# Optimization experiments

Hardware: AMD Instinct MI355X
Metric: run time of the kernel (lower is better)

## Reference

```python
import jax, jax.numpy as jnp
import numpy as np

D_MODEL = 1024
N_QK = 32
D_QK = 32
N_OV = 2048
D_OV = 1
SEQ = 1024
BATCH = 2
VKV = 16
ROT_DIM = 32
ROT_BASE = 10000.0
SCALE = D_QK ** 0.5  # cfg.attn_scale default = sqrt(d_qk_head)


def _kaiming(k, shape, fan_in):
    # torch kaiming_normal_(mode='fan_in', nonlinearity='relu'): std = sqrt(2/fan_in)
    return jax.random.normal(k, shape, jnp.float32) * np.sqrt(2.0 / fan_in)


def setup_inputs() -> dict:
    key = jax.random.key(0)
    ks = jax.random.split(key, 7)
    return {
        'resid': jax.random.normal(ks[0], (BATCH, SEQ, D_MODEL), jnp.float32),
        'W_Q': _kaiming(ks[1], (N_QK, D_MODEL, D_QK), D_MODEL * D_QK),
        'W_K': _kaiming(ks[2], (N_QK, D_MODEL, D_QK), D_MODEL * D_QK),
        'W_V': _kaiming(ks[3], (N_OV, D_MODEL, D_OV), D_MODEL * D_OV),
        'W_O': _kaiming(ks[4], (N_OV, D_OV, D_MODEL), D_OV * D_MODEL),
        'b_Q': jnp.zeros((N_QK, D_QK), jnp.float32),
        'b_K': jnp.zeros((N_QK, D_QK), jnp.float32),
        'b_V': jnp.zeros((N_OV, D_OV), jnp.float32),
        'virtual_k': _kaiming(ks[5], (VKV, N_QK, D_QK), N_QK * D_QK),
        'virtual_v': jnp.zeros((VKV, N_OV, D_OV), jnp.float32),
    }


def _rotary_sin_cos(n_ctx, rd, base):
    # GPT-NeoX style (non-adjacent pairs): freq repeated as (2 d)
    pos = jnp.arange(n_ctx, dtype=jnp.float32)
    dim = jnp.arange(rd // 2, dtype=jnp.float32)
    freq = base ** (dim / (rd / 2))
    freq = jnp.concatenate([freq, freq])
    angles = pos[:, None] / freq[None, :]  # (n_ctx, rd)
    return jnp.sin(angles), jnp.cos(angles)


def _apply_rotary(x, sin, cos, rd):
    # x: (batch, seq, head, d_head)
    s = x.shape[1]
    x_rot, x_pass = x[..., :rd], x[..., rd:]
    flip = jnp.concatenate([-x_rot[..., rd // 2:], x_rot[..., :rd // 2]], axis=-1)
    rot = x_rot * cos[None, :s, None, :] + flip * sin[None, :s, None, :]
    return jnp.concatenate([rot, x_pass], axis=-1)


def reference(resid, W_Q, W_K, W_V, W_O, b_Q, b_K, b_V, virtual_k, virtual_v):
    b, s, _ = resid.shape
    # per-head QKV projections + biases
    q = jnp.einsum('bsm,hmd->bshd', resid, W_Q) + b_Q  # (b,s,n_qk,d_qk)
    k = jnp.einsum('bsm,hmd->bshd', resid, W_K) + b_K
    v = jnp.einsum('bsm,hmd->bshd', resid, W_V) + b_V  # (b,s,n_ov,d_ov)
    sin, cos = _rotary_sin_cos(s, ROT_DIM, ROT_BASE)
    q = _apply_rotary(q, sin, cos, ROT_DIM)
    k = _apply_rotary(k, sin, cos, ROT_DIM)
    # append virtual KV at the end of the key axis
    k = jnp.concatenate([k, jnp.broadcast_to(virtual_k[None], (b,) + virtual_k.shape)], axis=1)
    v = jnp.concatenate([v, jnp.broadcast_to(virtual_v[None], (b,) + virtual_v.shape)], axis=1)
    kv_len = s + VKV
    scores = jnp.einsum('bqhd,bkhd->bhqk', q, k) / SCALE
    # causal mask: tril(ones(n_ctx, n_ctx+vkv), diagonal=vkv)
    mask = jnp.arange(kv_len)[None, :] <= (jnp.arange(s)[:, None] + VKV)
    scores = jnp.where(mask[None, None], scores, -jnp.inf)
    pattern = jax.nn.softmax(scores, axis=-1)
    pattern = jnp.where(jnp.isnan(pattern), 0.0, pattern)
    # repeat_interleave of pattern over ov heads == grouping v per qk head
    ratio = N_OV // N_QK
    v_g = v.reshape(b, kv_len, N_QK, ratio * D_OV)
    z = jnp.einsum('bhqk,bkhr->bqhr', pattern, v_g)  # (b,s,n_qk,ratio*d_ov)
    z = z.reshape(b, s, N_OV, D_OV)
    out = jnp.einsum('bqhd,hdm->bqm', z, W_O)  # cal_out: no b_O
    return out
```

## Files before the change

### kernel.cpp

```cpp
#include <hip/hip_runtime.h>
#include <hip/hip_bf16.h>
#include <math.h>


typedef short bf16x8 __attribute__((ext_vector_type(8)));
typedef short short4v __attribute__((ext_vector_type(4)));
typedef float f32x4 __attribute__((ext_vector_type(4)));
typedef int int4v __attribute__((ext_vector_type(4)));
typedef __hip_bfloat16 bf16;

#define AS1(p) ((const __attribute__((address_space(1))) void*)(const void*)(p))
#define AS3(p) ((__attribute__((address_space(3))) void*)(void*)(p))

static constexpr float INV_SCALE = 0.17677669529663687f;

__device__ inline short rnd_bf16(float x) {
  unsigned u = __float_as_uint(x);
  return (short)((u + 0x7fffu + ((u >> 16) & 1u)) >> 16);
}

__device__ inline int pack_bf16_pair(float hi, float lo) {
  unsigned a = __float_as_uint(hi) + 0x8000u;
  unsigned b = __float_as_uint(lo) + 0x8000u;
  return (int)__builtin_amdgcn_perm(a, b, 0x07060302u);
}

__global__ __launch_bounds__(256) void prep(
    const float* __restrict__ resid, const float* __restrict__ WV,
    const float* __restrict__ WQ, const float* __restrict__ WK,
    const float* __restrict__ WO, const float* __restrict__ vk,
    const float* __restrict__ vv,
    bf16* __restrict__ A_bf, bf16* __restrict__ Wt, bf16* __restrict__ Wot,
    bf16* __restrict__ Kb, bf16* __restrict__ Vb) {
  __shared__ float t[64][65];
  const int blk = blockIdx.x, tid = threadIdx.x;
  if (blk < 4096) {
    const float* src = (blk < 2048) ? resid : WV;
    short* dst = (short*)((blk < 2048) ? A_bf : (Wt + (size_t)2048 * 1024));
    int i = ((blk & 2047) * 256 + tid) * 4;
    float4 v = *(const float4*)(src + i);
    dst[i + 0] = rnd_bf16(v.x); dst[i + 1] = rnd_bf16(v.y);
    dst[i + 2] = rnd_bf16(v.z); dst[i + 3] = rnd_bf16(v.w);
  } else if (blk < 7168) {
    int idx = (blk - 4096) * 256 + tid;
    if (idx < 262144) {
      int b = idx >> 17, rem = idx & 131071;
      int j = rem >> 10, c = rem & 1023;
      int h = c >> 5, d = c & 31;
      float v = (j < 16) ? vk[j * 1024 + c] : 0.f;
      Kb[(((size_t)(b * 32 + h)) * 1152 + 1024 + j) * 32 + d] = __float2bfloat16(v);
    } else if (idx < 524288) {
      int i2 = idx - 262144;
      int b = i2 >> 17, rem = i2 & 131071;
      int ch = rem >> 6, p = rem & 63;
      int pl = p & 31;
      int u = (p & 32) | ((pl & 4) << 2) | ((pl & 24) >> 1) | (pl & 3);
      float v = (u < 16) ? vv[(size_t)u * 2048 + ch] : 0.f;
      int hv = ch >> 6, c = ch & 63;
      int slot = c * 8 + ((p >> 3) ^ (c & 7));
      Vb[((((size_t)(b * 32 + hv)) * 17 + 16) * 512 + slot) * 8 + (p & 7)] = __float2bfloat16(v);
    }
  } else if (blk < 8192) {
    int i = blk - 7168;
    int mt = i & 15, h = (i >> 4) & 31, qk = i >> 9;
    const float* W = qk ? WK : WQ;
    const int m0 = mt * 64;
    for (int idx = tid; idx < 64 * 32; idx += 256) {
      int ii = idx >> 5, d = idx & 31;
      t[ii][d] = W[((size_t)h * 1024 + m0 + ii) * 32 + d];
    }
    __syncthreads();
    const int rowbase = qk * 1024 + h * 32;
    for (int idx = tid; idx < 32 * 64; idx += 256) {
      int d = idx >> 6, ii = idx & 63;
      Wt[(size_t)(rowbase + d) * 1024 + m0 + ii] = __float2bfloat16(t[ii][d]);
    }
  } else {
    int i = blk - 8192;
    int h0 = (i & 31) * 64, m0 = (i >> 5) * 64;
    for (int idx = tid; idx < 64 * 64; idx += 256) {
      int ii = idx >> 6, j = idx & 63;
      t[ii][j] = WO[(size_t)(h0 + ii) * 1024 + m0 + j];
    }
    __syncthreads();
    for (int idx = tid; idx < 64 * 64; idx += 256) {
      int ii = idx >> 6, j = idx & 63;
      Wot[(size_t)(m0 + ii) * 2048 + h0 + j] = __float2bfloat16(t[j][ii]);
    }
  }
}

__global__ __launch_bounds__(256) void gemm1_fused(
    const bf16* __restrict__ A, const bf16* __restrict__ Bt,
    const float* __restrict__ bQ, const float* __restrict__ bK,
    const float* __restrict__ bV,
    bf16* __restrict__ Qb, bf16* __restrict__ Kb, bf16* __restrict__ Vb) {
  __shared__ __align__(16) short As[128 * 32];
  __shared__ __align__(16) short Bs[128 * 32];
  const int tileM = blockIdx.y * 128, tileN = blockIdx.x * 128;
  const int tid = threadIdx.x, wave = tid >> 6, lane = tid & 63;
  const int wm = (wave >> 1) * 64, wn = (wave & 1) * 64;
  const int mrow = lane & 15, kq = lane >> 4;
  f32x4 acc[4][4] = {};

  for (int k0 = 0; k0 < 1024; k0 += 32) {
#pragma unroll
    for (int i = 0; i < 2; i++) {
      int c = (wave * 2 + i) * 64 + lane;
      int row = c >> 2, ko = (c & 3) * 8;
      const short* ga = (const short*)A + (size_t)(tileM + row) * 1024 + k0 + ko;
      const short* gb = (const short*)Bt + (size_t)(tileN + row) * 1024 + k0 + ko;
      __builtin_amdgcn_global_load_lds(AS1(ga), AS3(&As[(wave * 2 + i) * 512]), 16, 0, 0);
      __builtin_amdgcn_global_load_lds(AS1(gb), AS3(&Bs[(wave * 2 + i) * 512]), 16, 0, 0);
    }
    __syncthreads();
    bf16x8 af[4], bfr[4];
#pragma unroll
    for (int t = 0; t < 4; t++) {
      af[t]  = *(const bf16x8*)&As[(wm + t * 16 + mrow) * 32 + kq * 8];
      bfr[t] = *(const bf16x8*)&Bs[(wn + t * 16 + mrow) * 32 + kq * 8];
    }
#pragma unroll
    for (int i = 0; i < 4; i++)
#pragma unroll
      for (int j = 0; j < 4; j++)
        acc[i][j] = __builtin_amdgcn_mfma_f32_16x16x32_bf16(af[i], bfr[j], acc[i][j], 0, 0, 0);
    __syncthreads();
  }

  const int col = lane & 15, rq = lane >> 4;
  if (tileN < 2048) {
    const int qk = tileN >> 10;
    const float* bias = qk ? bK : bQ;
    const int hA = ((tileN & 1023) + wn) >> 5;
    const float b0a = bias[hA * 32 + col],        b1a = bias[hA * 32 + col + 16];
    const float b0b = bias[(hA + 1) * 32 + col],  b1b = bias[(hA + 1) * 32 + col + 16];
    const float invf = exp2f(col * -0.8304820237218406f);
#pragma unroll
    for (int i = 0; i < 4; i++)
#pragma unroll
      for (int r = 0; r < 4; r++) {
        int mg = tileM + wm + i * 16 + rq * 4 + r;
        int s = mg & 1023, bb = mg >> 10;
        float sv, cv;
        __sincosf((float)s * invf, &sv, &cv);
#pragma unroll
        for (int p = 0; p < 2; p++) {
          float x0 = acc[i][2 * p][r]     + (p ? b0b : b0a);
          float x1 = acc[i][2 * p + 1][r] + (p ? b1b : b1a);
          float y0 = x0 * cv - x1 * sv, y1 = x1 * cv + x0 * sv;
          int h = hA + p;
          if (qk == 0) {
            short* q = (short*)Qb + (((size_t)(bb * 32 + h)) * 1024 + s) * 32 + col;
            q[0]  = rnd_bf16(y0 * INV_SCALE);
            q[16] = rnd_bf16(y1 * INV_SCALE);
          } else {
            short* kp = (short*)Kb + (((size_t)(bb * 32 + h)) * 1152 + s) * 32 + col;
            kp[0]  = rnd_bf16(y0);
            kp[16] = rnd_bf16(y1);
          }
        }
      }
  } else {
    const int hv = (tileN - 2048 + wn) >> 6;
#pragma unroll
    for (int i = 0; i < 4; i++)
#pragma unroll
      for (int j = 0; j < 4; j++) {
        int c = j * 16 + col;
        float bias = bV[hv * 64 + c];
        int m0 = tileM + wm + i * 16 + rq * 4;
        int s0 = m0 & 1023, bb = m0 >> 10;
        int chunk = s0 >> 6, w = s0 & 63, u0 = w & 31;
        int p0 = (u0 & 3) | ((u0 & 16) >> 2) | ((u0 & 8) << 1) | ((u0 & 4) << 1);
        int p = (w & 32) | p0;
        int slot = c * 8 + ((p >> 3) ^ (c & 7));
        short4v s4;
#pragma unroll
        for (int r = 0; r < 4; r++) s4[r] = rnd_bf16(acc[i][j][r] + bias);
        *(short4v*)((short*)Vb +
            ((((size_t)(bb * 32 + hv)) * 17 + chunk) * 512 + slot) * 8 + (p & 7)) = s4;
      }
  }
}

__global__ __launch_bounds__(256) void attn_mfma(
    const bf16* __restrict__ Qb, const bf16* __restrict__ Kb,
    const bf16* __restrict__ Vb, bf16* __restrict__ Zb) {
  __shared__ __align__(16) short Vs[4][4096];
  const int flat = blockIdx.x;
  const int xcd = flat & 7, jj = flat >> 3;
  const int hqb = xcd * 8 + (jj & 7);
  const int x = jj >> 3;
  const int hq = hqb & 31, b = hqb >> 5;
  const int wave = threadIdx.x >> 6, lane = threadIdx.x & 63;
  const int col = lane & 15, quad = lane >> 4;
  const int t = (wave == 0) ? x : (wave == 1) ? 31 - x : (wave == 2) ? 32 + x : 63 - x;
  const int qw = t * 16;

  const bf16x8 qf = *(const bf16x8*)((const short*)Qb +
      (((size_t)(b * 32 + hq)) * 1024 + qw + col) * 32 + quad * 8);
  const short* kbase = (const short*)Kb + ((size_t)(b * 32 + hq)) * 1152 * 32 + quad * 8;
  const short* vbh = (const short*)Vb + ((size_t)(b * 32 + hq)) * (17 * 4096) + lane * 8;
  short* vdst = &Vs[wave][0];

  const int kend = (qw + 32 < 1040) ? qw + 32 : 1040;
  const int nch = (kend + 63) >> 6;

  f32x4 O[4] = {};
  float m = -1e30f, l = 0.f;

  bf16x8 kf[4];
#pragma unroll
  for (int mbk = 0; mbk < 4; mbk++)
    kf[mbk] = *(const bf16x8*)(kbase + (size_t)(mbk * 16 + col) * 32);
#pragma unroll
  for (int g = 0; g < 8; g++)
    __builtin_amdgcn_global_load_lds(AS1(vbh + g * 512), AS3(vdst + g * 512), 16, 0, 0);

  for (int ci = 0; ci < nch; ci++) {
    const int kc = ci * 64;
    f32x4 St[4] = {};
#pragma unroll
    for (int mbk = 0; mbk < 4; mbk++)
      St[mbk] = __builtin_amdgcn_mfma_f32_16x16x32_bf16(kf[mbk], qf, St[mbk], 0, 0, 0);
    if (kc + 63 > qw + 16) {
      int qv = qw + col + 16;
#pragma unroll
      for (int mbk = 0; mbk < 4; mbk++)
#pragma unroll
        for (int r = 0; r < 4; r++)
          if (kc + mbk * 16 + quad * 4 + r > qv) St[mbk][r] = -1e30f;
    }
    float cm0 = fmaxf(fmaxf(St[0][0], St[0][1]), fmaxf(St[0][2], St[0][3]));
    float cm1 = fmaxf(fmaxf(St[1][0], St[1][1]), fmaxf(St[1][2], St[1][3]));
    float cm2 = fmaxf(fmaxf(St[2][0], St[2][1]), fmaxf(St[2][2], St[2][3]));
    float cm3 = fmaxf(fmaxf(St[3][0], St[3][1]), fmaxf(St[3][2], St[3][3]));
    float cmax = fmaxf(fmaxf(cm0, cm1), fmaxf(cm2, cm3));
    cmax = fmaxf(cmax, __shfl_xor(cmax, 16));
    cmax = fmaxf(cmax, __shfl_xor(cmax, 32));
    float mn = fmaxf(m, cmax);
    float al = __expf(m - mn);
    m = mn;
    float ps = 0.f;
#pragma unroll
    for (int mbk = 0; mbk < 4; mbk++)
#pragma unroll
      for (int r = 0; r < 4; r++) {
        float p = __expf(St[mbk][r] - mn);
        ps += p;
        St[mbk][r] = p;
      }
    ps += __shfl_xor(ps, 16);
    ps += __shfl_xor(ps, 32);
    l = l * al + ps;
    int4v pi[2];
#pragma unroll
    for (int pr = 0; pr < 2; pr++)
#pragma unroll
      for (int d = 0; d < 4; d++)
        pi[pr][d] = pack_bf16_pair(St[2 * pr + (d >> 1)][(d & 1) * 2 + 1],
                                   St[2 * pr + (d >> 1)][(d & 1) * 2]);
#pragma unroll
    for (int cb = 0; cb < 4; cb++)
#pragma unroll
      for (int r = 0; r < 4; r++) O[cb][r] *= al;
    asm volatile("s_waitcnt vmcnt(0)" ::: "memory");
    bf16x8 vf[2][4];
#pragma unroll
    for (int ks = 0; ks < 2; ks++)
#pragma unroll
      for (int cb = 0; cb < 4; cb++) {
        int slot = (cb * 16 + col) * 8 + ((ks * 4 + quad) ^ (col & 7));
        vf[ks][cb] = *(const bf16x8*)(vdst + slot * 8);
      }
    asm volatile("s_waitcnt lgkmcnt(0)" ::: "memory");
    if (ci + 1 < nch) {
      const int kn = kc + 64;
#pragma unroll
      for (int mbk = 0; mbk < 4; mbk++)
        kf[mbk] = *(const bf16x8*)(kbase + (size_t)(kn + mbk * 16 + col) * 32);
      const short* vsrc = vbh + (ci + 1) * 4096;
#pragma unroll
      for (int g = 0; g < 8; g++)
        __builtin_amdgcn_global_load_lds(AS1(vsrc + g * 512), AS3(vdst + g * 512), 16, 0, 0);
    }
#pragma unroll
    for (int ks = 0; ks < 2; ks++) {
      bf16x8 prs = *(bf16x8*)&pi[ks];
#pragma unroll
      for (int cb = 0; cb < 4; cb++)
        O[cb] = __builtin_amdgcn_mfma_f32_16x16x32_bf16(vf[ks][cb], prs, O[cb], 0, 0, 0);
    }
  }
  float inv = 1.f / l;
  short* zrow = (short*)Zb + ((size_t)(b * 1024 + qw + col)) * 2048 + hq * 64 + quad * 4;
#pragma unroll
  for (int cb = 0; cb < 4; cb++) {
    short4v s4;
#pragma unroll
    for (int r = 0; r < 4; r++) s4[r] = rnd_bf16(O[cb][r] * inv);
    *(short4v*)(zrow + cb * 16) = s4;
  }
}

__global__ __launch_bounds__(256) void gemm2_small(
    const bf16* __restrict__ A, const bf16* __restrict__ Bt, float* __restrict__ C,
    int K, int ldc) {
  __shared__ __align__(16) short As[64 * 32];
  __shared__ __align__(16) short Bs[64 * 32];
  const int tileM = blockIdx.y * 64, tileN = blockIdx.x * 64;
  const int tid = threadIdx.x, wave = tid >> 6, lane = tid & 63;
  const int wm = (wave >> 1) * 32, wn = (wave & 1) * 32;
  const int mrow = lane & 15, kq = lane >> 4;
  f32x4 acc[2][2] = {};

  for (int k0 = 0; k0 < K; k0 += 32) {
    {
      int c = wave * 64 + lane;
      int row = c >> 2, ko = (c & 3) * 8;
      const short* ga = (const short*)A + (size_t)(tileM + row) * K + k0 + ko;
      __builtin_amdgcn_global_load_lds(AS1(ga), AS3(&As[wave * 512]), 16, 0, 0);
    }
    {
      int c = wave * 64 + lane;
      int row = c >> 2, ko = (c & 3) * 8;
      const short* gb = (const short*)Bt + (size_t)(tileN + row) * K + k0 + ko;
      __builtin_amdgcn_global_load_lds(AS1(gb), AS3(&Bs[wave * 512]), 16, 0, 0);
    }
    __syncthreads();
    bf16x8 af[2], bfr[2];
#pragma unroll
    for (int t = 0; t < 2; t++) {
      af[t]  = *(const bf16x8*)&As[(wm + t * 16 + mrow) * 32 + kq * 8];
      bfr[t] = *(const bf16x8*)&Bs[(wn + t * 16 + mrow) * 32 + kq * 8];
    }
#pragma unroll
    for (int i = 0; i < 2; i++)
#pragma unroll
      for (int j = 0; j < 2; j++)
        acc[i][j] = __builtin_amdgcn_mfma_f32_16x16x32_bf16(af[i], bfr[j], acc[i][j], 0, 0, 0);
    __syncthreads();
  }
  const int col = lane & 15, rq = lane >> 4;
#pragma unroll
  for (int i = 0; i < 2; i++)
#pragma unroll
    for (int j = 0; j < 2; j++)
#pragma unroll
      for (int r = 0; r < 4; r++) {
        int mm = tileM + wm + i * 16 + rq * 4 + r;
        int nn = tileN + wn + j * 16 + col;
        C[(size_t)mm * ldc + nn] = acc[i][j][r];
      }
}

extern "C" void kernel_launch(void* const* d_in, const int* in_sizes, int n_in,
                              void* d_out, int out_size, void* d_ws, size_t ws_size,
                              hipStream_t stream) {
  const float* resid = (const float*)d_in[0];
  const float* WQ = (const float*)d_in[1];
  const float* WK = (const float*)d_in[2];
  const float* WV = (const float*)d_in[3];
  const float* WO = (const float*)d_in[4];
  const float* bQ = (const float*)d_in[5];
  const float* bK = (const float*)d_in[6];
  const float* bV = (const float*)d_in[7];
  const float* vk = (const float*)d_in[8];
  const float* vv = (const float*)d_in[9];
  float* out = (float*)d_out;

  char* ws = (char*)d_ws;
  bf16* A_bf = (bf16*)(ws);
  bf16* Wt   = (bf16*)(ws + 4194304);
  bf16* Wot  = (bf16*)(ws + 12582912);
  bf16* Qb   = (bf16*)(ws + 16777216);
  bf16* Kb   = (bf16*)(ws + 20971520);
  bf16* Vb   = (bf16*)(ws + 25690112);
  bf16* Zb   = (bf16*)(ws + 35127296);

  prep<<<8704, 256, 0, stream>>>(resid, WV, WQ, WK, WO, vk, vv, A_bf, Wt, Wot, Kb, Vb);
  gemm1_fused<<<dim3(32, 16), 256, 0, stream>>>(A_bf, Wt, bQ, bK, bV, Qb, Kb, Vb);
  attn_mfma<<<1024, 256, 0, stream>>>(Qb, Kb, Vb, Zb);
  gemm2_small<<<dim3(16, 32), 256, 0, stream>>>(Zb, Wot, out, 2048, 1024);
}
```

Before: 179.3 us.

## Remap GEMM blocks per XCD, transpose QK MFMA for vector stores, widen GEMM2 tile

Both GEMMs now use a 1D grid whose block index is remapped so that blocks sharing the same M rows land on the same XCD, aiming to improve L2 reuse. The QK part of gemm1 swaps the MFMA operand order so each lane holds 4 consecutive head dimensions, which allows vectorized bias loads and 8-byte packed stores for the rotary Q/K output instead of scattered 2-byte stores. GEMM2 grows its tile from 64x64 to 128x64 for more reuse per block, at the cost of halving the block count to 256 and lowering parallelism.

```diff
diff --git a/kernel.cpp b/kernel.cpp
--- a/kernel.cpp
+++ b/kernel.cpp
@@ -97,10 +97,14 @@
     bf16* __restrict__ Qb, bf16* __restrict__ Kb, bf16* __restrict__ Vb) {
   __shared__ __align__(16) short As[128 * 32];
   __shared__ __align__(16) short Bs[128 * 32];
-  const int tileM = blockIdx.y * 128, tileN = blockIdx.x * 128;
+  const int flat = blockIdx.x;
+  const int xcd = flat & 7, idx = flat >> 3;
+  const int tileM = (xcd * 2 + (idx >> 5)) * 128;
+  const int tileN = (idx & 31) * 128;
   const int tid = threadIdx.x, wave = tid >> 6, lane = tid & 63;
   const int wm = (wave >> 1) * 64, wn = (wave & 1) * 64;
   const int mrow = lane & 15, kq = lane >> 4;
+  const bool isQK = tileN < 2048;
   f32x4 acc[4][4] = {};
 
   for (int k0 = 0; k0 < 1024; k0 += 32) {
@@ -120,47 +124,63 @@
       af[t]  = *(const bf16x8*)&As[(wm + t * 16 + mrow) * 32 + kq * 8];
       bfr[t] = *(const bf16x8*)&Bs[(wn + t * 16 + mrow) * 32 + kq * 8];
     }
-#pragma unroll
-    for (int i = 0; i < 4; i++)
-#pragma unroll
-      for (int j = 0; j < 4; j++)
-        acc[i][j] = __builtin_amdgcn_mfma_f32_16x16x32_bf16(af[i], bfr[j], acc[i][j], 0, 0, 0);
+    if (isQK) {
+#pragma unroll
+      for (int fj = 0; fj < 4; fj++)
+#pragma unroll
+        for (int ti = 0; ti < 4; ti++)
+          acc[fj][ti] = __builtin_amdgcn_mfma_f32_16x16x32_bf16(bfr[fj], af[ti], acc[fj][ti], 0, 0, 0);
+    } else {
+#pragma unroll
+      for (int i = 0; i < 4; i++)
+#pragma unroll
+        for (int j = 0; j < 4; j++)
+          acc[i][j] = __builtin_amdgcn_mfma_f32_16x16x32_bf16(af[i], bfr[j], acc[i][j], 0, 0, 0);
+    }
     __syncthreads();
   }
 
   const int col = lane & 15, rq = lane >> 4;
-  if (tileN < 2048) {
+  if (isQK) {
     const int qk = tileN >> 10;
     const float* bias = qk ? bK : bQ;
     const int hA = ((tileN & 1023) + wn) >> 5;
-    const float b0a = bias[hA * 32 + col],        b1a = bias[hA * 32 + col + 16];
-    const float b0b = bias[(hA + 1) * 32 + col],  b1b = bias[(hA + 1) * 32 + col + 16];
-    const float invf = exp2f(col * -0.8304820237218406f);
-#pragma unroll
-    for (int i = 0; i < 4; i++)
-#pragma unroll
-      for (int r = 0; r < 4; r++) {
-        int mg = tileM + wm + i * 16 + rq * 4 + r;
-        int s = mg & 1023, bb = mg >> 10;
-        float sv, cv;
-        __sincosf((float)s * invf, &sv, &cv);
-#pragma unroll
-        for (int p = 0; p < 2; p++) {
-          float x0 = acc[i][2 * p][r]     + (p ? b0b : b0a);
-          float x1 = acc[i][2 * p + 1][r] + (p ? b1b : b1a);
-          float y0 = x0 * cv - x1 * sv, y1 = x1 * cv + x0 * sv;
-          int h = hA + p;
-          if (qk == 0) {
-            short* q = (short*)Qb + (((size_t)(bb * 32 + h)) * 1024 + s) * 32 + col;
-            q[0]  = rnd_bf16(y0 * INV_SCALE);
-            q[16] = rnd_bf16(y1 * INV_SCALE);
-          } else {
-            short* kp = (short*)Kb + (((size_t)(bb * 32 + h)) * 1152 + s) * 32 + col;
-            kp[0]  = rnd_bf16(y0);
-            kp[16] = rnd_bf16(y1);
-          }
+    const int d0 = rq * 4;
+    const float4 bA0 = *(const float4*)&bias[hA * 32 + d0];
+    const float4 bA1 = *(const float4*)&bias[hA * 32 + 16 + d0];
+    const float4 bB0 = *(const float4*)&bias[(hA + 1) * 32 + d0];
+    const float4 bB1 = *(const float4*)&bias[(hA + 1) * 32 + 16 + d0];
+    float invf[4];
+#pragma unroll
+    for (int r = 0; r < 4; r++)
+      invf[r] = exp2f((d0 + r) * -0.8304820237218406f);
+    const float osc = qk ? 1.f : INV_SCALE;
+#pragma unroll
+    for (int ti = 0; ti < 4; ti++) {
+      int sg = tileM + wm + ti * 16 + col;
+      int s = sg & 1023, bb = sg >> 10;
+      float sv[4], cv[4];
+#pragma unroll
+      for (int r = 0; r < 4; r++) __sincosf((float)s * invf[r], &sv[r], &cv[r]);
+#pragma unroll
+      for (int p = 0; p < 2; p++) {
+        int h = hA + p;
+        short4v z0, z1;
+#pragma unroll
+        for (int r = 0; r < 4; r++) {
+          float x0 = acc[2 * p][ti][r]     + (p ? (&bB0.x)[r] : (&bA0.x)[r]);
+          float x1 = acc[2 * p + 1][ti][r] + (p ? (&bB1.x)[r] : (&bA1.x)[r]);
+          float y0 = (x0 * cv[r] - x1 * sv[r]) * osc;
+          float y1 = (x1 * cv[r] + x0 * sv[r]) * osc;
+          z0[r] = rnd_bf16(y0); z1[r] = rnd_bf16(y1);
         }
+        short* dst = qk
+            ? (short*)Kb + ((size_t)(bb * 32 + h) * 1152 + s) * 32
+            : (short*)Qb + ((size_t)(bb * 32 + h) * 1024 + s) * 32;
+        *(short4v*)(dst + d0) = z0;
+        *(short4v*)(dst + 16 + d0) = z1;
       }
+    }
   } else {
     const int hv = (tileN - 2048 + wn) >> 6;
 #pragma unroll
@@ -304,39 +324,41 @@
   }
 }
 
-__global__ __launch_bounds__(256) void gemm2_small(
-    const bf16* __restrict__ A, const bf16* __restrict__ Bt, float* __restrict__ C,
-    int K, int ldc) {
-  __shared__ __align__(16) short As[64 * 32];
+__global__ __launch_bounds__(256) void gemm2_wide(
+    const bf16* __restrict__ A, const bf16* __restrict__ Bt, float* __restrict__ C) {
+  __shared__ __align__(16) short As[128 * 32];
   __shared__ __align__(16) short Bs[64 * 32];
-  const int tileM = blockIdx.y * 64, tileN = blockIdx.x * 64;
+  const int flat = blockIdx.x;
+  const int xcd = flat & 7, idx = flat >> 3;
+  const int tileM = (xcd * 2 + (idx >> 4)) * 128;
+  const int tileN = (idx & 15) * 64;
   const int tid = threadIdx.x, wave = tid >> 6, lane = tid & 63;
-  const int wm = (wave >> 1) * 32, wn = (wave & 1) * 32;
+  const int wm = (wave >> 1) * 64, wn = (wave & 1) * 32;
   const int mrow = lane & 15, kq = lane >> 4;
-  f32x4 acc[2][2] = {};
-
-  for (int k0 = 0; k0 < K; k0 += 32) {
+  f32x4 acc[4][2] = {};
+
+  for (int k0 = 0; k0 < 2048; k0 += 32) {
+#pragma unroll
+    for (int i = 0; i < 2; i++) {
+      int c = (wave * 2 + i) * 64 + lane;
+      int row = c >> 2, ko = (c & 3) * 8;
+      const short* ga = (const short*)A + (size_t)(tileM + row) * 2048 + k0 + ko;
+      __builtin_amdgcn_global_load_lds(AS1(ga), AS3(&As[(wave * 2 + i) * 512]), 16, 0, 0);
+    }
     {
       int c = wave * 64 + lane;
       int row = c >> 2, ko = (c & 3) * 8;
-      const short* ga = (const short*)A + (size_t)(tileM + row) * K + k0 + ko;
-      __builtin_amdgcn_global_load_lds(AS1(ga), AS3(&As[wave * 512]), 16, 0, 0);
-    }
-    {
-      int c = wave * 64 + lane;
-      int row = c >> 2, ko = (c & 3) * 8;
-      const short* gb = (const short*)Bt + (size_t)(tileN + row) * K + k0 + ko;
+      const short* gb = (const short*)Bt + (size_t)(tileN + row) * 2048 + k0 + ko;
       __builtin_amdgcn_global_load_lds(AS1(gb), AS3(&Bs[wave * 512]), 16, 0, 0);
     }
     __syncthreads();
-    bf16x8 af[2], bfr[2];
-#pragma unroll
-    for (int t = 0; t < 2; t++) {
-      af[t]  = *(const bf16x8*)&As[(wm + t * 16 + mrow) * 32 + kq * 8];
-      bfr[t] = *(const bf16x8*)&Bs[(wn + t * 16 + mrow) * 32 + kq * 8];
-    }
-#pragma unroll
-    for (int i = 0; i < 2; i++)
+    bf16x8 af[4], bfr[2];
+#pragma unroll
+    for (int t = 0; t < 4; t++) af[t] = *(const bf16x8*)&As[(wm + t * 16 + mrow) * 32 + kq * 8];
+#pragma unroll
+    for (int t = 0; t < 2; t++) bfr[t] = *(const bf16x8*)&Bs[(wn + t * 16 + mrow) * 32 + kq * 8];
+#pragma unroll
+    for (int i = 0; i < 4; i++)
 #pragma unroll
       for (int j = 0; j < 2; j++)
         acc[i][j] = __builtin_amdgcn_mfma_f32_16x16x32_bf16(af[i], bfr[j], acc[i][j], 0, 0, 0);
@@ -344,14 +366,14 @@
   }
   const int col = lane & 15, rq = lane >> 4;
 #pragma unroll
-  for (int i = 0; i < 2; i++)
+  for (int i = 0; i < 4; i++)
 #pragma unroll
     for (int j = 0; j < 2; j++)
 #pragma unroll
       for (int r = 0; r < 4; r++) {
         int mm = tileM + wm + i * 16 + rq * 4 + r;
         int nn = tileN + wn + j * 16 + col;
-        C[(size_t)mm * ldc + nn] = acc[i][j][r];
+        C[(size_t)mm * 1024 + nn] = acc[i][j][r];
       }
 }
 
@@ -380,7 +402,7 @@
   bf16* Zb   = (bf16*)(ws + 35127296);
 
   prep<<<8704, 256, 0, stream>>>(resid, WV, WQ, WK, WO, vk, vv, A_bf, Wt, Wot, Kb, Vb);
-  gemm1_fused<<<dim3(32, 16), 256, 0, stream>>>(A_bf, Wt, bQ, bK, bV, Qb, Kb, Vb);
+  gemm1_fused<<<512, 256, 0, stream>>>(A_bf, Wt, bQ, bK, bV, Qb, Kb, Vb);
   attn_mfma<<<1024, 256, 0, stream>>>(Qb, Kb, Vb, Zb);
-  gemm2_small<<<dim3(16, 32), 256, 0, stream>>>(Zb, Wot, out, 2048, 1024);
-}
+  gemm2_wide<<<256, 256, 0, stream>>>(Zb, Wot, out);
+}
```

Result: slower. 183.7 us (+2.4%).
